# Optimization experiments

Measured on AMD Instinct MI355X. Metric: run time of the kernel, lower is better.

## Reference

```python
import jax, jax.numpy as jnp
import numpy as np

N, E, C, L, B = 40000, 640000, 128, 3, 64
EPS = 1e-5


def _layer_norm(h, g, b):
    m = h.mean(-1, keepdims=True)
    v = h.var(-1, keepdims=True)
    return (h - m) / jnp.sqrt(v + EPS) * g + b


def setup_inputs() -> dict:
    key = jax.random.key(0)
    ks = jax.random.split(key, 24)
    s = 0.05
    inp = {
        "x": jax.random.normal(ks[0], (N, C), jnp.float32),
        "edge_index": jax.random.randint(ks[1], (2, E), 0, N, dtype=jnp.int32),
        "batch": jnp.sort(jax.random.randint(ks[2], (N,), 0, B, dtype=jnp.int32)),
        # pre-scaler Linear(in=C -> hidden=C)
        "pre_w": jax.random.normal(ks[3], (C, C), jnp.float32) * s,
        "pre_b": jnp.zeros((C,), jnp.float32),
        # per-layer GCNConv weight/bias
        "conv_w": jax.random.normal(ks[4], (L, C, C), jnp.float32) * s,
        "conv_b": jnp.zeros((L, C), jnp.float32),
        # per-layer post-conv LayerNorm (applied for layers 0..L-2)
        "ln_g": jnp.ones((L, C), jnp.float32),
        "ln_b": jnp.zeros((L, C), jnp.float32),
        # per-layer FFN: lin1, lin2, LayerNorm
        "ffn_w1": jax.random.normal(ks[5], (L, C, C), jnp.float32) * s,
        "ffn_b1": jnp.zeros((L, C), jnp.float32),
        "ffn_w2": jax.random.normal(ks[6], (L, C, C), jnp.float32) * s,
        "ffn_b2": jnp.zeros((L, C), jnp.float32),
        "ffn_ln_g": jnp.ones((L, C), jnp.float32),
        "ffn_ln_b": jnp.zeros((L, C), jnp.float32),
        # classifier MLP: Linear(C,C)+ReLU+Linear(C,1)
        "cls_w1": jax.random.normal(ks[7], (C, C), jnp.float32) * s,
        "cls_b1": jnp.zeros((C,), jnp.float32),
        "cls_w2": jax.random.normal(ks[8], (C, 1), jnp.float32) * s,
        "cls_b2": jnp.zeros((1,), jnp.float32),
    }
    return inp


def reference(x, edge_index, batch, pre_w, pre_b, conv_w, conv_b, ln_g, ln_b,
              ffn_w1, ffn_b1, ffn_w2, ffn_b2, ffn_ln_g, ffn_ln_b,
              cls_w1, cls_b1, cls_w2, cls_b2):
    src, dst = edge_index[0], edge_index[1]
    # GCN symmetric normalization with self-loops: deg counts incoming edges + 1
    deg = jax.ops.segment_sum(jnp.ones((E,), x.dtype), dst, num_segments=N) + 1.0
    inv_sqrt = jax.lax.rsqrt(deg)                      # [N]
    norm_e = inv_sqrt[src] * inv_sqrt[dst]             # [E]
    self_norm = inv_sqrt * inv_sqrt                    # [N], 1/deg for self-loop

    h = x @ pre_w + pre_b                              # pre_scaler

    for i in range(L):
        layer_in = h
        hw = h @ conv_w[i]                             # [N,C]
        msg = hw[src] * norm_e[:, None]                # gather + scale [E,C]
        h = jax.ops.segment_sum(msg, dst, num_segments=N)
        h = h + hw * self_norm[:, None] + conv_b[i]    # self-loop + bias
        if i < L - 1:
            h = _layer_norm(h, ln_g[i], ln_b[i])       # norm
            h = jax.nn.relu(h)                         # act (act_first=False)
            h = h + layer_in                           # residual (dropout=0)
            # FFN: lin2(relu(lin1(h))) + h, then norm
            y = jax.nn.relu(h @ ffn_w1[i] + ffn_b1[i]) @ ffn_w2[i] + ffn_b2[i] + h
            h = _layer_norm(y, ffn_ln_g[i], ffn_ln_b[i])

    # global mean pool per graph
    counts = jax.ops.segment_sum(jnp.ones((N,), h.dtype), batch, num_segments=B)
    g = jax.ops.segment_sum(h, batch, num_segments=B) / jnp.maximum(counts, 1.0)[:, None]

    out = jax.nn.relu(g @ cls_w1 + cls_b1) @ cls_w2 + cls_b2   # [B,1]
    return out
```

## Files before the change

kernel.cpp:

```cpp
#include <hip/hip_runtime.h>
#include <hip/hip_fp16.h>
#include <cstdint>
#include <cstddef>

#define N_NODES 40000
#define N_EDGES 640000
#define CH 128
#define NL 3
#define NB 64
#define LN_EPS 1e-5f
#define TSTRIDE 132
#define GBLK 625
#define FBLK 2500

typedef short short8 __attribute__((ext_vector_type(8)));
typedef float floatx4 __attribute__((ext_vector_type(4)));

__device__ __forceinline__ unsigned short bf16_rne(float f) {
    unsigned int u = __float_as_uint(f);
    unsigned int r = u + 0x7FFF + ((u >> 16) & 1);
    return (unsigned short)(r >> 16);
}

__device__ __forceinline__ void lds_fence() {
    asm volatile("s_waitcnt lgkmcnt(0)" ::: "memory");
    __builtin_amdgcn_sched_barrier(0);
}

__launch_bounds__(256)
__global__ void degpack_kernel(const int* __restrict__ ei, int* __restrict__ degi,
                               const float* __restrict__ pre_w, const float* __restrict__ conv_w,
                               const float* __restrict__ ffn_w1, const float* __restrict__ ffn_w2,
                               short* __restrict__ wpk) {
    int bid = blockIdx.x;
    if (bid < FBLK) {
        int e = bid * 256 + threadIdx.x;
        atomicAdd(&degi[ei[N_EDGES + e]], 1);
        return;
    }
    int idx = (bid - FBLK) * 256 + threadIdx.x;
    int mat = idx >> 14;
    int e = idx & 16383;
    int k = e >> 7, n = e & 127;
    const float* src;
    switch (mat) {
        case 0: src = pre_w; break;
        case 1: case 2: case 3: src = conv_w + (size_t)(mat - 1) * 16384; break;
        case 4: case 5: src = ffn_w1 + (size_t)(mat - 4) * 16384; break;
        default: src = ffn_w2 + (size_t)(mat - 6) * 16384; break;
    }
    float f = src[e];
    unsigned short h = bf16_rne(f);
    float hf = __uint_as_float((unsigned)h << 16);
    unsigned short l = bf16_rne(f - hf);
    int kk = k >> 5, quad = (k >> 3) & 3, j = k & 7;
    int frag = ((kk * 4 + quad) * 128 + n) * 8 + j;
    wpk[(size_t)mat * 32768 + frag] = (short)h;
    wpk[(size_t)mat * 32768 + 16384 + frag] = (short)l;
}

__global__ void scan1_kernel(const int* __restrict__ degi, int* __restrict__ rowptr,
                             int* __restrict__ bsum, float* __restrict__ isq) {
    __shared__ int s[256];
    int t = threadIdx.x;
    int i = blockIdx.x * 256 + t;
    int v = (i < N_NODES) ? degi[i] : 0;
    if (i < N_NODES) isq[i] = rsqrtf((float)v + 1.0f);
    s[t] = v;
    __syncthreads();
    for (int off = 1; off < 256; off <<= 1) {
        int add = (t >= off) ? s[t - off] : 0;
        __syncthreads();
        s[t] += add;
        __syncthreads();
    }
    if (i < N_NODES) rowptr[i + 1] = s[t];
    if (t == 255) bsum[blockIdx.x] = s[255];
}

__global__ void scan23_kernel(const int* __restrict__ bsum, int* __restrict__ rowptr, int nb) {
    __shared__ int s[256];
    int t = threadIdx.x;
    int v = (t < nb) ? bsum[t] : 0;
    s[t] = v;
    __syncthreads();
    for (int off = 1; off < 256; off <<= 1) {
        int add = (t >= off) ? s[t - off] : 0;
        __syncthreads();
        s[t] += add;
        __syncthreads();
    }
    int bid = blockIdx.x;
    int boff = (bid > 0) ? s[bid - 1] : 0;
    int i = bid * 256 + t;
    if (i < N_NODES) rowptr[i + 1] += boff;
    if (i == 0 && bid == 0) rowptr[0] = 0;
}


__device__ __forceinline__ void split8(const float* av, short8& ahi, short8& alo) {
#pragma unroll
    for (int j = 0; j < 8; ++j) {
        unsigned short hb = bf16_rne(av[j]);
        ahi[j] = (short)hb;
        alo[j] = (short)bf16_rne(av[j] - __uint_as_float((unsigned)hb << 16));
    }
}

__device__ __forceinline__ void bload_mfma2(const short* __restrict__ bh,
                                            short8 ahi0, short8 alo0,
                                            short8 ahi1, short8 alo1,
                                            floatx4* acc0, floatx4* acc1) {
    short8 bhi[8], blo[8];
#pragma unroll
    for (int c = 0; c < 8; ++c) {
        bhi[c] = *(const short8*)(bh + c * 128);
        blo[c] = *(const short8*)(bh + 16384 + c * 128);
    }
#pragma unroll
    for (int c = 0; c < 8; ++c) {
        acc0[c] = __builtin_amdgcn_mfma_f32_16x16x32_bf16(ahi0, bhi[c], acc0[c], 0, 0, 0);
        acc0[c] = __builtin_amdgcn_mfma_f32_16x16x32_bf16(alo0, bhi[c], acc0[c], 0, 0, 0);
        acc0[c] = __builtin_amdgcn_mfma_f32_16x16x32_bf16(ahi0, blo[c], acc0[c], 0, 0, 0);
        acc1[c] = __builtin_amdgcn_mfma_f32_16x16x32_bf16(ahi1, bhi[c], acc1[c], 0, 0, 0);
        acc1[c] = __builtin_amdgcn_mfma_f32_16x16x32_bf16(alo1, bhi[c], acc1[c], 0, 0, 0);
        acc1[c] = __builtin_amdgcn_mfma_f32_16x16x32_bf16(ahi1, blo[c], acc1[c], 0, 0, 0);
    }
}

template <int VARIANT>
__device__ __forceinline__ void gemm_core(int tid, int bid,
                                          const float* __restrict__ A, const short* __restrict__ W1pk,
                                          const float* __restrict__ b1, const short* __restrict__ W2pk,
                                          const float* __restrict__ b2, const float* __restrict__ Res,
                                          const float* __restrict__ gamma, const float* __restrict__ beta,
                                          const short* __restrict__ W3pk,
                                          float* __restrict__ OutG, __half* __restrict__ OutC) {
    __shared__ float tbuf[64 * TSTRIDE];
    const int lane = tid & 63;
    const int wv = tid >> 6;
    const int row0 = bid * 64 + wv * 32;
    const int m = lane & 15;
    const int quad = lane >> 4;

    floatx4 acc[2][8];
#pragma unroll
    for (int t = 0; t < 2; ++t)
#pragma unroll
        for (int c = 0; c < 8; ++c) acc[t][c] = (floatx4){0.f, 0.f, 0.f, 0.f};

    const float* arow0 = A + (size_t)(row0 + m) * CH + quad * 8;
    const float* arow1 = arow0 + (size_t)16 * CH;
    float* trow_w = tbuf + (wv * 32) * TSTRIDE;
    const float* trow0 = tbuf + (wv * 32 + m) * TSTRIDE + quad * 8;
    const float* trow1 = trow0 + 16 * TSTRIDE;
    const int boff = quad * 1024 + m * 8;

#pragma unroll
    for (int kk = 0; kk < 4; ++kk) {
        float4 a0 = *(const float4*)(arow0 + kk * 32);
        float4 a1 = *(const float4*)(arow0 + kk * 32 + 4);
        float4 a2 = *(const float4*)(arow1 + kk * 32);
        float4 a3 = *(const float4*)(arow1 + kk * 32 + 4);
        float av0[8] = {a0.x, a0.y, a0.z, a0.w, a1.x, a1.y, a1.z, a1.w};
        float av1[8] = {a2.x, a2.y, a2.z, a2.w, a3.x, a3.y, a3.z, a3.w};
        short8 ahi0, alo0, ahi1, alo1;
        split8(av0, ahi0, alo0);
        split8(av1, ahi1, alo1);
        bload_mfma2(W1pk + kk * 4096 + boff, ahi0, alo0, ahi1, alo1, acc[0], acc[1]);
    }

#pragma unroll
    for (int t = 0; t < 2; ++t)
#pragma unroll
    for (int c = 0; c < 8; ++c) {
        int col = c * 16 + m;
        float bv = b1[col];
#pragma unroll
        for (int r = 0; r < 4; ++r) {
            int lrow = t * 16 + quad * 4 + r;
            float v = acc[t][c][r] + bv;
            if (VARIANT == 1) v = fmaxf(v, 0.f);
            trow_w[lrow * TSTRIDE + col] = v;
            if (VARIANT == 0)
                OutG[(size_t)(row0 + lrow) * CH + col] = v;
        }
        acc[t][c] = (floatx4){0.f, 0.f, 0.f, 0.f};
    }
    lds_fence();

#pragma unroll
    for (int kk = 0; kk < 4; ++kk) {
        float av0[8], av1[8];
#pragma unroll
        for (int j = 0; j < 8; ++j) av0[j] = trow0[kk * 32 + j];
#pragma unroll
        for (int j = 0; j < 8; ++j) av1[j] = trow1[kk * 32 + j];
        short8 ahi0, alo0, ahi1, alo1;
        split8(av0, ahi0, alo0);
        split8(av1, ahi1, alo1);
        bload_mfma2(W2pk + kk * 4096 + boff, ahi0, alo0, ahi1, alo1, acc[0], acc[1]);
    }

    if (VARIANT == 0) {
#pragma unroll
        for (int t = 0; t < 2; ++t)
#pragma unroll
        for (int c = 0; c < 8; ++c) {
            int col = c * 16 + m;
#pragma unroll
            for (int r = 0; r < 4; ++r) {
                int row = row0 + t * 16 + quad * 4 + r;
                OutC[(size_t)row * CH + col] = __float2half(acc[t][c][r]);
            }
        }
        return;
    }

#pragma unroll
    for (int t = 0; t < 2; ++t)
#pragma unroll
    for (int c = 0; c < 8; ++c) {
        int col = c * 16 + m;
        float bv = b2[col];
#pragma unroll
        for (int r = 0; r < 4; ++r)
            acc[t][c][r] += bv + Res[(size_t)(row0 + t * 16 + quad * 4 + r) * CH + col];
    }
#pragma unroll
    for (int t = 0; t < 2; ++t)
#pragma unroll
    for (int r = 0; r < 4; ++r) {
        float s = 0.f, q = 0.f;
#pragma unroll
        for (int c = 0; c < 8; ++c) {
            float v = acc[t][c][r];
            s += v;
            q = fmaf(v, v, q);
        }
#pragma unroll
        for (int msk = 1; msk < 16; msk <<= 1) {
            s += __shfl_xor(s, msk);
            q += __shfl_xor(q, msk);
        }
        float mean = s * (1.f / CH);
        float var = q * (1.f / CH) - mean * mean;
        float rstd = rsqrtf(var + LN_EPS);
        int lrow = t * 16 + quad * 4 + r;
        int row = row0 + lrow;
#pragma unroll
        for (int c = 0; c < 8; ++c) {
            int col = c * 16 + m;
            float y = (acc[t][c][r] - mean) * rstd * gamma[col] + beta[col];
            OutG[(size_t)row * CH + col] = y;
            trow_w[lrow * TSTRIDE + col] = y;
        }
    }
#pragma unroll
    for (int t = 0; t < 2; ++t)
#pragma unroll
    for (int c = 0; c < 8; ++c) acc[t][c] = (floatx4){0.f, 0.f, 0.f, 0.f};
    lds_fence();

#pragma unroll
    for (int kk = 0; kk < 4; ++kk) {
        float av0[8], av1[8];
#pragma unroll
        for (int j = 0; j < 8; ++j) av0[j] = trow0[kk * 32 + j];
#pragma unroll
        for (int j = 0; j < 8; ++j) av1[j] = trow1[kk * 32 + j];
        short8 ahi0, alo0, ahi1, alo1;
        split8(av0, ahi0, alo0);
        split8(av1, ahi1, alo1);
        bload_mfma2(W3pk + kk * 4096 + boff, ahi0, alo0, ahi1, alo1, acc[0], acc[1]);
    }

#pragma unroll
    for (int t = 0; t < 2; ++t)
#pragma unroll
    for (int c = 0; c < 8; ++c) {
        int col = c * 16 + m;
#pragma unroll
        for (int r = 0; r < 4; ++r) {
            int row = row0 + t * 16 + quad * 4 + r;
            OutC[(size_t)row * CH + col] = __float2half(acc[t][c][r]);
        }
    }
}

template <int VARIANT>
__launch_bounds__(128, 2)
__global__ void gemm_fused(const float* __restrict__ A, const short* __restrict__ W1pk,
                           const float* __restrict__ b1, const short* __restrict__ W2pk,
                           const float* __restrict__ b2, const float* __restrict__ Res,
                           const float* __restrict__ gamma, const float* __restrict__ beta,
                           const short* __restrict__ W3pk,
                           float* __restrict__ OutG, __half* __restrict__ OutC) {
    gemm_core<VARIANT>(threadIdx.x, blockIdx.x, A, W1pk, b1, W2pk, b2, Res,
                       gamma, beta, W3pk, OutG, OutC);
}

__launch_bounds__(256, 2)
__global__ void fillgemm0_kernel(const int* __restrict__ ei, const int* __restrict__ rowptr,
                                 int* __restrict__ fill, int* __restrict__ srcs,
                                 const float* __restrict__ A, const short* __restrict__ W1pk,
                                 const float* __restrict__ b1, const short* __restrict__ W2pk,
                                 float* __restrict__ OutG, __half* __restrict__ OutC) {
    int bid = blockIdx.x;
    if (bid < GBLK) {
        if (threadIdx.x >= 128) return;
        gemm_core<0>(threadIdx.x, bid, A, W1pk, b1, W2pk, nullptr, nullptr,
                     nullptr, nullptr, nullptr, OutG, OutC);
        return;
    }
    int e = (bid - GBLK) * 256 + threadIdx.x;
    int s = ei[e];
    int d = ei[N_EDGES + e];
    int pos = atomicAdd(&fill[d], 1);
    srcs[rowptr[d] + pos] = s;
}

template <int FUSED>
__launch_bounds__(256)
__global__ void agg_kernel(const __half* __restrict__ HW, const int* __restrict__ rowptr,
                           const int* __restrict__ srcs, const float* __restrict__ isq,
                           const float* __restrict__ bias, const float* __restrict__ gamma,
                           const float* __restrict__ beta, float* __restrict__ Hres,
                           float* __restrict__ Out) {
    const int lane = threadIdx.x & 63;
    const int node = blockIdx.x * 4 + (threadIdx.x >> 6);
    const int start = rowptr[node];
    const int end = rowptr[node + 1];

    float ax = 0.f, ay = 0.f;
    for (int base = start; base < end; base += 64) {
        int idx = base + lane;
        int clamped = (idx < end) ? idx : (end - 1);
        int sl = srcs[clamped];
        float wl = isq[sl];
        int cnt = end - base;
        if (cnt > 64) cnt = 64;
        int j = 0;
        for (; j + 8 <= cnt; j += 8) {
            int s[8];
            float w[8];
            float2 v[8];
#pragma unroll
            for (int q = 0; q < 8; ++q) {
                s[q] = __shfl(sl, j + q);
                w[q] = __shfl(wl, j + q);
            }
#pragma unroll
            for (int q = 0; q < 8; ++q)
                v[q] = __half22float2(*(const __half2*)(HW + (size_t)s[q] * CH + lane * 2));
#pragma unroll
            for (int q = 0; q < 8; ++q) {
                ax = fmaf(w[q], v[q].x, ax);
                ay = fmaf(w[q], v[q].y, ay);
            }
        }
        for (; j + 4 <= cnt; j += 4) {
            int s0 = __shfl(sl, j), s1 = __shfl(sl, j + 1);
            int s2 = __shfl(sl, j + 2), s3 = __shfl(sl, j + 3);
            float w0 = __shfl(wl, j), w1 = __shfl(wl, j + 1);
            float w2 = __shfl(wl, j + 2), w3 = __shfl(wl, j + 3);
            float2 v0 = __half22float2(*(const __half2*)(HW + (size_t)s0 * CH + lane * 2));
            float2 v1 = __half22float2(*(const __half2*)(HW + (size_t)s1 * CH + lane * 2));
            float2 v2 = __half22float2(*(const __half2*)(HW + (size_t)s2 * CH + lane * 2));
            float2 v3 = __half22float2(*(const __half2*)(HW + (size_t)s3 * CH + lane * 2));
            ax = fmaf(w0, v0.x, ax); ay = fmaf(w0, v0.y, ay);
            ax = fmaf(w1, v1.x, ax); ay = fmaf(w1, v1.y, ay);
            ax = fmaf(w2, v2.x, ax); ay = fmaf(w2, v2.y, ay);
            ax = fmaf(w3, v3.x, ax); ay = fmaf(w3, v3.y, ay);
        }
        for (; j < cnt; ++j) {
            int s = __shfl(sl, j);
            float w = __shfl(wl, j);
            float2 vf = __half22float2(*(const __half2*)(HW + (size_t)s * CH + lane * 2));
            ax = fmaf(w, vf.x, ax);
            ay = fmaf(w, vf.y, ay);
        }
    }
    float d = isq[node];
    const __half2 hv = *(const __half2*)(HW + (size_t)node * CH + lane * 2);
    float2 hf = __half22float2(hv);
    const float2 bb = *(const float2*)(bias + lane * 2);
    float hx = d * ax + d * d * hf.x + bb.x;
    float hy = d * ay + d * d * hf.y + bb.y;

    if (!FUSED) {
        float2 o; o.x = hx; o.y = hy;
        *(float2*)(Out + (size_t)node * CH + lane * 2) = o;
        return;
    }
    float sum = hx + hy;
    float sq = hx * hx + hy * hy;
    for (int msk = 1; msk < 64; msk <<= 1) {
        sum += __shfl_xor(sum, msk);
        sq += __shfl_xor(sq, msk);
    }
    float mean = sum * (1.f / CH);
    float var = sq * (1.f / CH) - mean * mean;
    float rstd = rsqrtf(var + LN_EPS);
    const float2 gg = *(const float2*)(gamma + lane * 2);
    const float2 be = *(const float2*)(beta + lane * 2);
    float y0 = (hx - mean) * rstd * gg.x + be.x;
    float y1 = (hy - mean) * rstd * gg.y + be.y;
    float2* hp = (float2*)(Hres + (size_t)node * CH + lane * 2);
    float2 rr = *hp;
    float2 o;
    o.x = fmaxf(y0, 0.f) + rr.x;
    o.y = fmaxf(y1, 0.f) + rr.y;
    *hp = o;
}

__launch_bounds__(256)
__global__ void pool_kernel(const float* __restrict__ H, const int* __restrict__ batch,
                            float* __restrict__ g, float* __restrict__ cntf) {
    const int lane = threadIdx.x & 63;
    const int w = blockIdx.x * 4 + (threadIdx.x >> 6);
    const int n0 = w * 16;
    float lx = 0.f, ly = 0.f;
    int run = 0;
    int cur = batch[n0];
    for (int t = 0; t < 16; ++t) {
        int n = n0 + t;
        int b = batch[n];
        if (b != cur) {
            atomicAdd(&g[(size_t)cur * CH + lane * 2], lx);
            atomicAdd(&g[(size_t)cur * CH + lane * 2 + 1], ly);
            if (lane == 0) atomicAdd(&cntf[cur], (float)run);
            lx = ly = 0.f; run = 0; cur = b;
        }
        const float2 v = *(const float2*)(H + (size_t)n * CH + lane * 2);
        lx += v.x; ly += v.y; ++run;
    }
    atomicAdd(&g[(size_t)cur * CH + lane * 2], lx);
    atomicAdd(&g[(size_t)cur * CH + lane * 2 + 1], ly);
    if (lane == 0) atomicAdd(&cntf[cur], (float)run);
}

__launch_bounds__(128)
__global__ void cls_kernel(const float* __restrict__ g, const float* __restrict__ cntf,
                           const float* __restrict__ w1, const float* __restrict__ b1,
                           const float* __restrict__ w2, const float* __restrict__ b2,
                           float* __restrict__ out) {
    __shared__ float gm[CH];
    __shared__ float red[2];
    const int b = blockIdx.x;
    const int t = threadIdx.x;
    float inv = 1.f / fmaxf(cntf[b], 1.f);
    gm[t] = g[(size_t)b * CH + t] * inv;
    __syncthreads();
    float acc = b1[t];
    for (int k = 0; k < CH; ++k) acc = fmaf(gm[k], w1[(size_t)k * CH + t], acc);
    float v = fmaxf(acc, 0.f) * w2[t];
    for (int msk = 1; msk < 64; msk <<= 1) v += __shfl_xor(v, msk);
    if ((t & 63) == 0) red[t >> 6] = v;
    __syncthreads();
    if (t == 0) out[b] = red[0] + red[1] + b2[0];
}


extern "C" void kernel_launch(void* const* d_in, const int* in_sizes, int n_in,
                              void* d_out, int out_size, void* d_ws, size_t ws_size,
                              hipStream_t stream) {
    const float* x      = (const float*)d_in[0];
    const int*   ei     = (const int*)d_in[1];
    const int*   batch  = (const int*)d_in[2];
    const float* pre_w  = (const float*)d_in[3];
    const float* pre_b  = (const float*)d_in[4];
    const float* conv_w = (const float*)d_in[5];
    const float* conv_b = (const float*)d_in[6];
    const float* ln_g   = (const float*)d_in[7];
    const float* ln_b   = (const float*)d_in[8];
    const float* ffn_w1 = (const float*)d_in[9];
    const float* ffn_b1 = (const float*)d_in[10];
    const float* ffn_w2 = (const float*)d_in[11];
    const float* ffn_b2 = (const float*)d_in[12];
    const float* fln_g  = (const float*)d_in[13];
    const float* fln_b  = (const float*)d_in[14];
    const float* cls_w1 = (const float*)d_in[15];
    const float* cls_b1 = (const float*)d_in[16];
    const float* cls_w2 = (const float*)d_in[17];
    const float* cls_b2 = (const float*)d_in[18];

    float* H    = (float*)d_ws;
    float* T    = H + (size_t)N_NODES * CH;
    float* R    = T + (size_t)N_NODES * CH;
    __half* HWh = (__half*)R;
    int*   degi = (int*)(R + (size_t)N_NODES * CH);
    int*   fill = degi + N_NODES;
    float* g    = (float*)(fill + N_NODES);
    float* cntf = g + (size_t)NB * CH;
    float* isq  = cntf + NB;
    int*  rowptr = (int*)(isq + N_NODES);
    int*  bsum   = rowptr + N_NODES + 1;
    int*  boff   = bsum + 256;
    int*  srcs   = boff + 256;
    short* wpk   = (short*)(srcs + N_EDGES);

    const int nb_scan = (N_NODES + 255) / 256;

    hipMemsetAsync(degi, 0, (size_t)(2 * N_NODES + NB * CH + NB) * sizeof(int), stream);

    degpack_kernel<<<FBLK + 512, 256, 0, stream>>>(ei, degi, pre_w, conv_w,
                                                   ffn_w1, ffn_w2, wpk);
    scan1_kernel<<<nb_scan, 256, 0, stream>>>(degi, rowptr, bsum, isq);
    scan23_kernel<<<nb_scan, 256, 0, stream>>>(bsum, rowptr, nb_scan);
    fillgemm0_kernel<<<GBLK + FBLK, 256, 0, stream>>>(ei, rowptr, fill, srcs,
                                                      x, wpk, pre_b,
                                                      wpk + 1 * 32768, H, HWh);

    const int lblk = N_NODES / 4;

    for (int i = 0; i < NL; ++i) {
        if (i < NL - 1) {
            agg_kernel<1><<<lblk, 256, 0, stream>>>(HWh, rowptr, srcs, isq,
                                                    conv_b + (size_t)i * CH,
                                                    ln_g + (size_t)i * CH,
                                                    ln_b + (size_t)i * CH, H, nullptr);
            gemm_fused<1><<<GBLK, 128, 0, stream>>>(H, wpk + (size_t)(4 + i) * 32768,
                                                    ffn_b1 + (size_t)i * CH,
                                                    wpk + (size_t)(6 + i) * 32768,
                                                    ffn_b2 + (size_t)i * CH, H,
                                                    fln_g + (size_t)i * CH,
                                                    fln_b + (size_t)i * CH,
                                                    wpk + (size_t)(2 + i) * 32768,
                                                    H, HWh);
        } else {
            agg_kernel<0><<<lblk, 256, 0, stream>>>(HWh, rowptr, srcs, isq,
                                                    conv_b + (size_t)i * CH,
                                                    nullptr, nullptr, nullptr, T);
        }
    }

    pool_kernel<<<N_NODES / 64, 256, 0, stream>>>(T, batch, g, cntf);
    cls_kernel<<<NB, CH, 0, stream>>>(g, cntf, cls_w1, cls_b1, cls_w2, cls_b2,
                                      (float*)d_out);
}
```

Measured before the change: 339.3 us.

## Aggregate each node with 16 lanes using 16-byte half loads

The aggregation kernel now assigns 16 lanes per node instead of a full 64-lane wavefront. Each lane loads 8 fp16 channels with one 16-byte load and keeps 8 accumulators, so each block covers 16 nodes and the LayerNorm reduction only spans 16 lanes. This is meant to cut instruction and shuffle overhead per gathered row and give more independent nodes per wave, at the cost of more registers. The GEMM k-loops are also set to not unroll, which lowers register pressure but may hurt instruction scheduling.

```diff
diff --git a/kernel.cpp b/kernel.cpp
--- a/kernel.cpp
+++ b/kernel.cpp
@@ -156,7 +156,7 @@
     const float* trow1 = trow0 + 16 * TSTRIDE;
     const int boff = quad * 1024 + m * 8;
 
-#pragma unroll
+#pragma unroll 1
     for (int kk = 0; kk < 4; ++kk) {
         float4 a0 = *(const float4*)(arow0 + kk * 32);
         float4 a1 = *(const float4*)(arow0 + kk * 32 + 4);
@@ -189,7 +189,7 @@
     }
     lds_fence();
 
-#pragma unroll
+#pragma unroll 1
     for (int kk = 0; kk < 4; ++kk) {
         float av0[8], av1[8];
 #pragma unroll
@@ -262,7 +262,7 @@
     for (int c = 0; c < 8; ++c) acc[t][c] = (floatx4){0.f, 0.f, 0.f, 0.f};
     lds_fence();
 
-#pragma unroll
+#pragma unroll 1
     for (int kk = 0; kk < 4; ++kk) {
         float av0[8], av1[8];
 #pragma unroll
@@ -327,91 +327,144 @@
                            const float* __restrict__ bias, const float* __restrict__ gamma,
                            const float* __restrict__ beta, float* __restrict__ Hres,
                            float* __restrict__ Out) {
-    const int lane = threadIdx.x & 63;
-    const int node = blockIdx.x * 4 + (threadIdx.x >> 6);
+    const int sub = threadIdx.x & 15;
+    const int node = blockIdx.x * 16 + (threadIdx.x >> 4);
     const int start = rowptr[node];
     const int end = rowptr[node + 1];
 
-    float ax = 0.f, ay = 0.f;
-    for (int base = start; base < end; base += 64) {
-        int idx = base + lane;
+    float a0 = 0.f, a1 = 0.f, a2 = 0.f, a3 = 0.f;
+    float a4 = 0.f, a5 = 0.f, a6 = 0.f, a7 = 0.f;
+    for (int base = start; base < end; base += 16) {
+        int idx = base + sub;
         int clamped = (idx < end) ? idx : (end - 1);
         int sl = srcs[clamped];
         float wl = isq[sl];
         int cnt = end - base;
-        if (cnt > 64) cnt = 64;
+        if (cnt > 16) cnt = 16;
         int j = 0;
         for (; j + 8 <= cnt; j += 8) {
             int s[8];
             float w[8];
-            float2 v[8];
+            float4 pk[8];
 #pragma unroll
             for (int q = 0; q < 8; ++q) {
-                s[q] = __shfl(sl, j + q);
-                w[q] = __shfl(wl, j + q);
+                s[q] = __shfl(sl, j + q, 16);
+                w[q] = __shfl(wl, j + q, 16);
             }
 #pragma unroll
             for (int q = 0; q < 8; ++q)
-                v[q] = __half22float2(*(const __half2*)(HW + (size_t)s[q] * CH + lane * 2));
+                pk[q] = *(const float4*)(HW + (size_t)s[q] * CH + sub * 8);
 #pragma unroll
             for (int q = 0; q < 8; ++q) {
-                ax = fmaf(w[q], v[q].x, ax);
-                ay = fmaf(w[q], v[q].y, ay);
+                float2 fa = __half22float2(*(const __half2*)&pk[q].x);
+                float2 fb = __half22float2(*(const __half2*)&pk[q].y);
+                float2 fc = __half22float2(*(const __half2*)&pk[q].z);
+                float2 fd = __half22float2(*(const __half2*)&pk[q].w);
+                a0 = fmaf(w[q], fa.x, a0); a1 = fmaf(w[q], fa.y, a1);
+                a2 = fmaf(w[q], fb.x, a2); a3 = fmaf(w[q], fb.y, a3);
+                a4 = fmaf(w[q], fc.x, a4); a5 = fmaf(w[q], fc.y, a5);
+                a6 = fmaf(w[q], fd.x, a6); a7 = fmaf(w[q], fd.y, a7);
             }
         }
         for (; j + 4 <= cnt; j += 4) {
-            int s0 = __shfl(sl, j), s1 = __shfl(sl, j + 1);
-            int s2 = __shfl(sl, j + 2), s3 = __shfl(sl, j + 3);
-            float w0 = __shfl(wl, j), w1 = __shfl(wl, j + 1);
-            float w2 = __shfl(wl, j + 2), w3 = __shfl(wl, j + 3);
-            float2 v0 = __half22float2(*(const __half2*)(HW + (size_t)s0 * CH + lane * 2));
-            float2 v1 = __half22float2(*(const __half2*)(HW + (size_t)s1 * CH + lane * 2));
-            float2 v2 = __half22float2(*(const __half2*)(HW + (size_t)s2 * CH + lane * 2));
-            float2 v3 = __half22float2(*(const __half2*)(HW + (size_t)s3 * CH + lane * 2));
-            ax = fmaf(w0, v0.x, ax); ay = fmaf(w0, v0.y, ay);
-            ax = fmaf(w1, v1.x, ax); ay = fmaf(w1, v1.y, ay);
-            ax = fmaf(w2, v2.x, ax); ay = fmaf(w2, v2.y, ay);
-            ax = fmaf(w3, v3.x, ax); ay = fmaf(w3, v3.y, ay);
+            int s[4];
+            float w[4];
+            float4 pk[4];
+#pragma unroll
+            for (int q = 0; q < 4; ++q) {
+                s[q] = __shfl(sl, j + q, 16);
+                w[q] = __shfl(wl, j + q, 16);
+            }
+#pragma unroll
+            for (int q = 0; q < 4; ++q)
+                pk[q] = *(const float4*)(HW + (size_t)s[q] * CH + sub * 8);
+#pragma unroll
+            for (int q = 0; q < 4; ++q) {
+                float2 fa = __half22float2(*(const __half2*)&pk[q].x);
+                float2 fb = __half22float2(*(const __half2*)&pk[q].y);
+                float2 fc = __half22float2(*(const __half2*)&pk[q].z);
+                float2 fd = __half22float2(*(const __half2*)&pk[q].w);
+                a0 = fmaf(w[q], fa.x, a0); a1 = fmaf(w[q], fa.y, a1);
+                a2 = fmaf(w[q], fb.x, a2); a3 = fmaf(w[q], fb.y, a3);
+                a4 = fmaf(w[q], fc.x, a4); a5 = fmaf(w[q], fc.y, a5);
+                a6 = fmaf(w[q], fd.x, a6); a7 = fmaf(w[q], fd.y, a7);
+            }
         }
         for (; j < cnt; ++j) {
-            int s = __shfl(sl, j);
-            float w = __shfl(wl, j);
-            float2 vf = __half22float2(*(const __half2*)(HW + (size_t)s * CH + lane * 2));
-            ax = fmaf(w, vf.x, ax);
-            ay = fmaf(w, vf.y, ay);
+            int s = __shfl(sl, j, 16);
+            float w = __shfl(wl, j, 16);
+            float4 p = *(const float4*)(HW + (size_t)s * CH + sub * 8);
+            float2 fa = __half22float2(*(const __half2*)&p.x);
+            float2 fb = __half22float2(*(const __half2*)&p.y);
+            float2 fc = __half22float2(*(const __half2*)&p.z);
+            float2 fd = __half22float2(*(const __half2*)&p.w);
+            a0 = fmaf(w, fa.x, a0); a1 = fmaf(w, fa.y, a1);
+            a2 = fmaf(w, fb.x, a2); a3 = fmaf(w, fb.y, a3);
+            a4 = fmaf(w, fc.x, a4); a5 = fmaf(w, fc.y, a5);
+            a6 = fmaf(w, fd.x, a6); a7 = fmaf(w, fd.y, a7);
         }
     }
     float d = isq[node];
-    const __half2 hv = *(const __half2*)(HW + (size_t)node * CH + lane * 2);
-    float2 hf = __half22float2(hv);
-    const float2 bb = *(const float2*)(bias + lane * 2);
-    float hx = d * ax + d * d * hf.x + bb.x;
-    float hy = d * ay + d * d * hf.y + bb.y;
+    float4 hp8 = *(const float4*)(HW + (size_t)node * CH + sub * 8);
+    float2 ha = __half22float2(*(const __half2*)&hp8.x);
+    float2 hb = __half22float2(*(const __half2*)&hp8.y);
+    float2 hc = __half22float2(*(const __half2*)&hp8.z);
+    float2 hd = __half22float2(*(const __half2*)&hp8.w);
+    const float4 bb0 = *(const float4*)(bias + sub * 8);
+    const float4 bb1 = *(const float4*)(bias + sub * 8 + 4);
+    float h0 = d * a0 + d * d * ha.x + bb0.x;
+    float h1 = d * a1 + d * d * ha.y + bb0.y;
+    float h2 = d * a2 + d * d * hb.x + bb0.z;
+    float h3 = d * a3 + d * d * hb.y + bb0.w;
+    float h4 = d * a4 + d * d * hc.x + bb1.x;
+    float h5 = d * a5 + d * d * hc.y + bb1.y;
+    float h6 = d * a6 + d * d * hd.x + bb1.z;
+    float h7 = d * a7 + d * d * hd.y + bb1.w;
 
     if (!FUSED) {
-        float2 o; o.x = hx; o.y = hy;
-        *(float2*)(Out + (size_t)node * CH + lane * 2) = o;
+        float4 o0, o1;
+        o0.x = h0; o0.y = h1; o0.z = h2; o0.w = h3;
+        o1.x = h4; o1.y = h5; o1.z = h6; o1.w = h7;
+        *(float4*)(Out + (size_t)node * CH + sub * 8) = o0;
+        *(float4*)(Out + (size_t)node * CH + sub * 8 + 4) = o1;
         return;
     }
-    float sum = hx + hy;
-    float sq = hx * hx + hy * hy;
-    for (int msk = 1; msk < 64; msk <<= 1) {
+    float sum = ((h0 + h1) + (h2 + h3)) + ((h4 + h5) + (h6 + h7));
+    float sq = ((h0 * h0 + h1 * h1) + (h2 * h2 + h3 * h3)) +
+               ((h4 * h4 + h5 * h5) + (h6 * h6 + h7 * h7));
+    for (int msk = 1; msk < 16; msk <<= 1) {
         sum += __shfl_xor(sum, msk);
         sq += __shfl_xor(sq, msk);
     }
     float mean = sum * (1.f / CH);
     float var = sq * (1.f / CH) - mean * mean;
     float rstd = rsqrtf(var + LN_EPS);
-    const float2 gg = *(const float2*)(gamma + lane * 2);
-    const float2 be = *(const float2*)(beta + lane * 2);
-    float y0 = (hx - mean) * rstd * gg.x + be.x;
-    float y1 = (hy - mean) * rstd * gg.y + be.y;
-    float2* hp = (float2*)(Hres + (size_t)node * CH + lane * 2);
-    float2 rr = *hp;
-    float2 o;
-    o.x = fmaxf(y0, 0.f) + rr.x;
-    o.y = fmaxf(y1, 0.f) + rr.y;
-    *hp = o;
+    const float4 gg0 = *(const float4*)(gamma + sub * 8);
+    const float4 gg1 = *(const float4*)(gamma + sub * 8 + 4);
+    const float4 be0 = *(const float4*)(beta + sub * 8);
+    const float4 be1 = *(const float4*)(beta + sub * 8 + 4);
+    float y0 = (h0 - mean) * rstd * gg0.x + be0.x;
+    float y1 = (h1 - mean) * rstd * gg0.y + be0.y;
+    float y2 = (h2 - mean) * rstd * gg0.z + be0.z;
+    float y3 = (h3 - mean) * rstd * gg0.w + be0.w;
+    float y4 = (h4 - mean) * rstd * gg1.x + be1.x;
+    float y5 = (h5 - mean) * rstd * gg1.y + be1.y;
+    float y6 = (h6 - mean) * rstd * gg1.z + be1.z;
+    float y7 = (h7 - mean) * rstd * gg1.w + be1.w;
+    float4* hp0 = (float4*)(Hres + (size_t)node * CH + sub * 8);
+    float4* hp1 = (float4*)(Hres + (size_t)node * CH + sub * 8 + 4);
+    float4 r0 = *hp0, r1 = *hp1;
+    float4 o0, o1;
+    o0.x = fmaxf(y0, 0.f) + r0.x;
+    o0.y = fmaxf(y1, 0.f) + r0.y;
+    o0.z = fmaxf(y2, 0.f) + r0.z;
+    o0.w = fmaxf(y3, 0.f) + r0.w;
+    o1.x = fmaxf(y4, 0.f) + r1.x;
+    o1.y = fmaxf(y5, 0.f) + r1.y;
+    o1.z = fmaxf(y6, 0.f) + r1.z;
+    o1.w = fmaxf(y7, 0.f) + r1.w;
+    *hp0 = o0;
+    *hp1 = o1;
 }
 
 __launch_bounds__(256)
@@ -512,11 +565,11 @@
                                                       x, wpk, pre_b,
                                                       wpk + 1 * 32768, H, HWh);
 
-    const int lblk = N_NODES / 4;
+    const int ablk = N_NODES / 16;
 
     for (int i = 0; i < NL; ++i) {
         if (i < NL - 1) {
-            agg_kernel<1><<<lblk, 256, 0, stream>>>(HWh, rowptr, srcs, isq,
+            agg_kernel<1><<<ablk, 256, 0, stream>>>(HWh, rowptr, srcs, isq,
                                                     conv_b + (size_t)i * CH,
                                                     ln_g + (size_t)i * CH,
                                                     ln_b + (size_t)i * CH, H, nullptr);
@@ -529,7 +582,7 @@
                                                     wpk + (size_t)(2 + i) * 32768,
                                                     H, HWh);
         } else {
-            agg_kernel<0><<<lblk, 256, 0, stream>>>(HWh, rowptr, srcs, isq,
+            agg_kernel<0><<<ablk, 256, 0, stream>>>(HWh, rowptr, srcs, isq,
                                                     conv_b + (size_t)i * CH,
                                                     nullptr, nullptr, nullptr, T);
         }
```

Result: no change. 344.2 us (+1.4%).
